# Performance work log

Hardware: AMD Instinct MI355X
Metric: run time of the kernel (lower is better)

The kernel has to match this reference:

```python
import jax, jax.numpy as jnp
import numpy as np

G = 4          # conv groups (hardcoded in module)
C = 1024       # channels (hardcoded cin=cout=1024)
SCALE = 1.0 / np.sqrt(1024.0).astype(np.float32)  # 1/sqrt(c/h), h=1


def grouped_proj(x, W, b):
    # pointwise grouped Conv1d == block-diagonal matmul over channel groups
    # x: [B, C, P], W: [G, C//G out, C//G in], b: [C]
    B, C_, P = x.shape
    xg = x.reshape(B, G, C_ // G, P)
    y = jnp.einsum('goi,bgip->bgop', W, xg)  # [B, G, C//G, P]
    return y.reshape(B, C_, P) + b[None, :, None]


def setup_inputs() -> dict:
    key = jax.random.key(0)
    ks = jax.random.split(key, 8)
    B, PK, PQ = 8, 1024, 4096
    cg = C // G
    w_std = 1.0 / np.sqrt(cg).astype(np.float32)  # ~ conv default init scale
    return {
        'Xq': jax.random.normal(ks[0], (B, C, PQ), jnp.float32),
        'Xk': jax.random.normal(ks[1], (B, C, PK), jnp.float32),
        'Wq': jax.random.normal(ks[2], (G, cg, cg), jnp.float32) * w_std,
        'bq': jax.random.normal(ks[3], (C,), jnp.float32) * 0.01,
        'Wk': jax.random.normal(ks[4], (G, cg, cg), jnp.float32) * w_std,
        'bk': jax.random.normal(ks[5], (C,), jnp.float32) * 0.01,
        'Wv': jax.random.normal(ks[6], (G, cg, cg), jnp.float32) * w_std,
        'bv': jax.random.normal(ks[7], (C,), jnp.float32) * 0.01,
    }


def reference(Xq, Xk, Wq, bq, Wk, bk, Wv, bv):
    # Q and K are both projected from Xk; V from Xq (as in the torch code)
    Q = grouped_proj(Xk, Wq, bq)   # [B, C, Pk]
    K = grouped_proj(Xk, Wk, bk)   # [B, C, Pk]
    V = grouped_proj(Xq, Wv, bv)   # [B, C, Pq]
    b, c, pk = K.shape
    pq = V.shape[-1]
    h = 1
    Qh = Q.reshape(b, h, c // h, pk)
    Kh = K.reshape(b, h, c // h, pk)
    Vh = V.reshape(b, h, c // h, pq)
    # H: [B, h, Pk, Pq], contraction over channels; softmax over dim=-2 (Pk)
    H = jnp.einsum('bhci,bhcj->bhij', Kh, Vh) * SCALE
    H = jax.nn.softmax(H, axis=-2)
    # sparse_constrain: Gram over last axis vs identity, mean squared error
    mid = jnp.einsum('bhci,bhki->bhck', H, H)          # [B, h, Pk, Pk]
    Iden = jnp.eye(pk, dtype=H.dtype)[None, None]       # broadcast over B, h
    sparse_loss = jnp.mean((mid - Iden) ** 2)
    # out: mix Q along Pk with attention H -> [B, h, C, Pq]
    out = jnp.einsum('bhij,bhki->bhkj', H, Qh).reshape(b, c, pq)
    return out, sparse_loss, H
```

## Files before the change

kernel.cpp:

```cpp
#include <hip/hip_runtime.h>

typedef _Float16 f16;
typedef f16 f16x8 __attribute__((ext_vector_type(8)));
typedef float f32x4 __attribute__((ext_vector_type(4)));

__device__ __forceinline__ void gload16(const void* g, void* ldsbase) {
  __builtin_amdgcn_global_load_lds((const __attribute__((address_space(1))) unsigned int*)g,
                                   (__attribute__((address_space(3))) unsigned int*)ldsbase, 16, 0, 0);
}

__device__ __forceinline__ int swz(int row, int c) {
  return row * 64 + ((c ^ ((row >> 1) & 3)) << 4);
}

template<int MODE>
__global__ void __launch_bounds__(512, 2)
gemm256(const f16* __restrict__ A, const f16* __restrict__ Bm, float* __restrict__ Cf,
        f16* __restrict__ E16, f16* __restrict__ E16t,
        int K, long sA, long sB, float scale, float* __restrict__ aux) {
  __shared__ f16 sb[65536];
  const int t = threadIdx.x, l = t & 63, w = t >> 6;
  const int wr = w >> 2, wc = w & 3;
  const int bid = blockIdx.x;
  const int swzb = (bid & 7) * 64 + (bid >> 3);
  const long b = swzb >> 6;
  const int by = (swzb >> 4) & 3, bx = swzb & 15;
  const char* Abyte = (const char*)(A + b * sA + (long)(by * 256) * K);
  const char* Bbyte = (const char*)(Bm + b * sB + (long)(bx * 256) * K);

  int offSrc[4];
#pragma unroll
  for (int i = 0; i < 4; ++i) {
    int cid = i * 512 + t, row = cid >> 3, slot = cid & 7;
    offSrc[i] = row * (K * 2) + ((slot ^ (row & 7)) << 4);
  }
  int offAf[8][2], offBf[4][2];
#pragma unroll
  for (int mi = 0; mi < 8; ++mi) {
    int r = wr * 128 + mi * 16 + (l & 15);
#pragma unroll
    for (int ks = 0; ks < 2; ++ks)
      offAf[mi][ks] = r * 64 + ((((ks << 2) + (l >> 4)) ^ (r & 7)) << 3);
  }
#pragma unroll
  for (int ni = 0; ni < 4; ++ni) {
    int r = wc * 64 + ni * 16 + (l & 15);
#pragma unroll
    for (int ks = 0; ks < 2; ++ks)
      offBf[ni][ks] = r * 64 + ((((ks << 2) + (l >> 4)) ^ (r & 7)) << 3);
  }

  const int NT = K >> 6;
  f32x4 acc[8][4] = {};

  auto STAGE = [&](int kt, int bsel) {
    f16* la = sb + bsel * 32768;
    f16* lb = la + 16384;
    const char* as = Abyte + (long)kt * 128;
    const char* bs = Bbyte + (long)kt * 128;
#pragma unroll
    for (int i = 0; i < 4; ++i)
      gload16(as + offSrc[i], la + (i * 512 + (w << 6)) * 8);
#pragma unroll
    for (int i = 0; i < 4; ++i)
      gload16(bs + offSrc[i], lb + (i * 512 + (w << 6)) * 8);
  };

  STAGE(0, 0);
  for (int kt = 0; kt < NT; ++kt) {
    const int cur = kt & 1;
    if (kt + 1 < NT) {
      STAGE(kt + 1, cur ^ 1);
      asm volatile("s_waitcnt vmcnt(8)" ::: "memory");
    } else {
      asm volatile("s_waitcnt vmcnt(0)" ::: "memory");
    }
    __builtin_amdgcn_s_barrier();
    asm volatile("" ::: "memory");
    const f16* la = sb + cur * 32768;
    const f16* lb = la + 16384;
#pragma unroll
    for (int ks = 0; ks < 2; ++ks) {
      f16x8 bf[4];
#pragma unroll
      for (int ni = 0; ni < 4; ++ni) bf[ni] = *(const f16x8*)(lb + offBf[ni][ks]);
#pragma unroll
      for (int mi = 0; mi < 8; ++mi) {
        f16x8 af = *(const f16x8*)(la + offAf[mi][ks]);
#pragma unroll
        for (int ni = 0; ni < 4; ++ni)
          acc[mi][ni] = __builtin_amdgcn_mfma_f32_16x16x32_f16(af, bf[ni], acc[mi][ni], 0, 0, 0);
      }
    }
    asm volatile("s_waitcnt lgkmcnt(0)" ::: "memory");
    __builtin_amdgcn_s_barrier();
    asm volatile("" ::: "memory");
  }

  const int i0 = by * 256, j0 = bx * 256;
  if (MODE == 2) {
    float csum[4] = {};
#pragma unroll
    for (int mi = 0; mi < 8; ++mi)
#pragma unroll
      for (int ni = 0; ni < 4; ++ni)
#pragma unroll
        for (int q = 0; q < 4; ++q) {
          float e = __expf(acc[mi][ni][q] * scale);
          acc[mi][ni][q] = e;
          csum[ni] += e;
        }
#pragma unroll
    for (int ni = 0; ni < 4; ++ni) {
      csum[ni] += __shfl_xor(csum[ni], 16);
      csum[ni] += __shfl_xor(csum[ni], 32);
    }
    float* colp = (float*)(sb + 34816);
    if (l < 16) {
#pragma unroll
      for (int ni = 0; ni < 4; ++ni) colp[wr * 256 + wc * 64 + ni * 16 + l] = csum[ni];
    }
    __syncthreads();
    if (t < 256) aux[(b * 4 + by) * 4096 + bx * 256 + t] = colp[t] + colp[256 + t];
    f16* E16b = E16 + b * 4194304L;
    f16* E16tb = E16t + b * 4194304L;
#pragma unroll
    for (int s = 0; s < 4; ++s) {
      if (wr == (s >> 1)) {
        const int h = s & 1;
#pragma unroll
        for (int m2 = 0; m2 < 4; ++m2)
#pragma unroll
          for (int ni = 0; ni < 4; ++ni)
#pragma unroll
            for (int q = 0; q < 4; ++q)
              sb[(m2 * 16 + (l >> 4) * 4 + q) * 264 + wc * 64 + ni * 16 + (l & 15)] =
                  (f16)acc[h * 4 + m2][ni][q];
      }
      __syncthreads();
#pragma unroll
      for (int ii = 0; ii < 4; ++ii) {
        int cid = ii * 512 + t, r = cid >> 5, cc = cid & 31;
        *(f16x8*)(E16b + (long)(i0 + s * 64 + r) * 4096 + j0 + cc * 8) =
            *(const f16x8*)(sb + r * 264 + cc * 8);
      }
      const int q4 = w >> 1, r8 = l >> 3, ic = l & 7;
#pragma unroll
      for (int ii = 0; ii < 4; ++ii) {
        int j = q4 * 64 + r8 * 8 + (w & 1) * 4 + ii;
        f16x8 v;
#pragma unroll
        for (int k2 = 0; k2 < 8; ++k2) v[k2] = sb[(ic * 8 + k2) * 264 + j];
        *(f16x8*)(E16tb + (long)(j0 + j) * 1024 + i0 + s * 64 + ic * 8) = v;
      }
      __syncthreads();
    }
  } else {
    const float* ip = aux + b * 4096 + bx * 256 + wc * 64;
    float iv[4];
#pragma unroll
    for (int ni = 0; ni < 4; ++ni) iv[ni] = ip[ni * 16 + (l & 15)];
    float* Cb = Cf + b * 4194304L + (long)(by * 256 + wr * 128) * 4096 + bx * 256 + wc * 64;
#pragma unroll
    for (int mi = 0; mi < 8; ++mi)
#pragma unroll
      for (int ni = 0; ni < 4; ++ni)
#pragma unroll
        for (int q = 0; q < 4; ++q)
          Cb[(long)(mi * 16 + (l >> 4) * 4 + q) * 4096 + ni * 16 + (l & 15)] = acc[mi][ni][q] * iv[ni];
  }
}

__global__ void __launch_bounds__(256, 2)
gram_p(const f16* __restrict__ E, const f16* __restrict__ inv16g, float* __restrict__ parts) {
  __shared__ f16 sb[36864];
  const int t = threadIdx.x, l = t & 63, w = t >> 6, wr = w >> 1, wc = w & 1;
  const int bid = blockIdx.x;
  const int swzb = (bid & 7) * 64 + (bid >> 3);
  const long b = swzb >> 6;
  const int by = (swzb >> 3) & 7, bx = swzb & 7;
  const char* Abyte = (const char*)(E + b * 4194304L + (long)(by * 128) * 4096);
  const char* Bbyte = (const char*)(E + b * 4194304L + (long)(bx * 128) * 4096);
  f16* invl = sb + 32768;
  {
    const char* ig = (const char*)(inv16g + b * 4096);
    gload16(ig + (long)t * 16, invl + (w << 6) * 8);
    gload16(ig + 4096 + (long)t * 16, invl + 2048 + (w << 6) * 8);
  }
  int offSrc[4];
#pragma unroll
  for (int i = 0; i < 4; ++i) {
    int cid = i * 256 + t, row = cid >> 3, slot = cid & 7;
    offSrc[i] = row * 8192 + ((slot ^ (row & 7)) << 4);
  }
  int offA[4][2], offB[4][2];
#pragma unroll
  for (int mi = 0; mi < 4; ++mi) {
    int ra = wr * 64 + mi * 16 + (l & 15);
    int rb = wc * 64 + mi * 16 + (l & 15);
#pragma unroll
    for (int ks = 0; ks < 2; ++ks) {
      offA[mi][ks] = ra * 64 + ((((ks << 2) + (l >> 4)) ^ (ra & 7)) << 3);
      offB[mi][ks] = rb * 64 + ((((ks << 2) + (l >> 4)) ^ (rb & 7)) << 3);
    }
  }
  auto STAGE = [&](int kt, int bsel) {
    f16* la = sb + bsel * 16384;
    f16* lb = la + 8192;
    const char* as = Abyte + (long)kt * 128;
    const char* bs = Bbyte + (long)kt * 128;
#pragma unroll
    for (int i = 0; i < 4; ++i) gload16(as + offSrc[i], la + (i * 256 + (w << 6)) * 8);
#pragma unroll
    for (int i = 0; i < 4; ++i) gload16(bs + offSrc[i], lb + (i * 256 + (w << 6)) * 8);
  };
  f32x4 acc[4][4] = {};
  STAGE(0, 0);
  for (int kt = 0; kt < 64; ++kt) {
    const int cur = kt & 1;
    if (kt + 1 < 64) {
      STAGE(kt + 1, cur ^ 1);
      asm volatile("s_waitcnt vmcnt(8)" ::: "memory");
    } else {
      asm volatile("s_waitcnt vmcnt(0)" ::: "memory");
    }
    __builtin_amdgcn_s_barrier();
    asm volatile("" ::: "memory");
    const f16* la = sb + cur * 16384;
    const f16* lb = la + 8192;
#pragma unroll
    for (int ks = 0; ks < 2; ++ks) {
      const f16x8 invv = *(const f16x8*)(invl + kt * 64 + ks * 32 + ((l >> 4) << 3));
      f16x8 bf[4];
#pragma unroll
      for (int ni = 0; ni < 4; ++ni) bf[ni] = *(const f16x8*)(lb + offB[ni][ks]) * invv;
#pragma unroll
      for (int mi = 0; mi < 4; ++mi) {
        f16x8 af = *(const f16x8*)(la + offA[mi][ks]) * invv;
#pragma unroll
        for (int ni = 0; ni < 4; ++ni)
          acc[mi][ni] = __builtin_amdgcn_mfma_f32_16x16x32_f16(af, bf[ni], acc[mi][ni], 0, 0, 0);
      }
    }
    asm volatile("s_waitcnt lgkmcnt(0)" ::: "memory");
    __builtin_amdgcn_s_barrier();
    asm volatile("" ::: "memory");
  }
  const int gr0 = by * 128 + wr * 64 + (l >> 4) * 4;
  const int gc0 = bx * 128 + wc * 64 + (l & 15);
  float p = 0.f;
#pragma unroll
  for (int mi = 0; mi < 4; ++mi)
#pragma unroll
    for (int ni = 0; ni < 4; ++ni)
#pragma unroll
      for (int q = 0; q < 4; ++q) {
        float e = acc[mi][ni][q];
        if (gr0 + mi * 16 + q == gc0 + ni * 16) e -= 1.f;
        p += e * e;
      }
#pragma unroll
  for (int d = 32; d; d >>= 1) p += __shfl_down(p, d);
  __shared__ float red[4];
  if (l == 0) red[w] = p;
  __syncthreads();
  if (t == 0) parts[bid] = red[0] + red[1] + red[2] + red[3];
}

__global__ void __launch_bounds__(256)
proj_q(const float* __restrict__ X, const f16* __restrict__ W16, const float* __restrict__ bias,
       f16* __restrict__ Q, int P) {
  __shared__ f16 As[4096], Bs[4096];
  const int t = threadIdx.x, l = t & 63, w = t >> 6, wr = w >> 1, wc = w & 1;
  const int bg = blockIdx.z, g = bg & 3;
  const long b = bg >> 2;
  const int p0 = blockIdx.x * 128, m0 = blockIdx.y * 128;
  const float* Xb = X + b * 1024 * P + (long)g * 256 * P;
  const f16* Wg = W16 + g * 65536 + m0 * 256;
  const int r0 = t >> 2, cs = (t & 3) ^ ((r0 >> 1) & 3);
  const f16* wS0 = Wg + r0 * 256 + cs * 8;
  const f16* wS1 = Wg + (r0 + 64) * 256 + cs * 8;
  const int xp = t & 63, xc = t >> 6;
  const float* xS = Xb + (long)(xc * 8) * P + p0 + xp;
  const int xo0 = swz(xp, xc), xo1 = swz(xp + 64, xc);
  int offA[4], offB[4];
#pragma unroll
  for (int i = 0; i < 4; ++i) {
    int ra = wr * 64 + i * 16 + (l & 15);
    offA[i] = swz(ra, l >> 4);
    int rb = wc * 64 + i * 16 + (l & 15);
    offB[i] = swz(rb, l >> 4);
  }
  f32x4 acc[4][4] = {};
  for (int k0 = 0; k0 < 256; k0 += 32) {
    gload16(wS0 + k0, As + w * 512);
    gload16(wS1 + k0, As + 2048 + w * 512);
    const float* xs = xS + (long)k0 * P;
    f16x8 v0, v1;
#pragma unroll
    for (int d = 0; d < 8; ++d) v0[d] = (f16)xs[(long)d * P];
#pragma unroll
    for (int d = 0; d < 8; ++d) v1[d] = (f16)xs[(long)d * P + 64];
    *(f16x8*)((char*)Bs + xo0) = v0;
    *(f16x8*)((char*)Bs + xo1) = v1;
    __syncthreads();
    f16x8 af[4], bf[4];
#pragma unroll
    for (int i = 0; i < 4; ++i) {
      af[i] = *(const f16x8*)((const char*)As + offA[i]);
      bf[i] = *(const f16x8*)((const char*)Bs + offB[i]);
    }
#pragma unroll
    for (int mi = 0; mi < 4; ++mi)
#pragma unroll
      for (int ni = 0; ni < 4; ++ni)
        acc[mi][ni] = __builtin_amdgcn_mfma_f32_16x16x32_f16(af[mi], bf[ni], acc[mi][ni], 0, 0, 0);
    __syncthreads();
  }
  f16* Qb = Q + b * 1048576 + (long)(g * 256 + m0 + wr * 64) * 1024 + p0 + wc * 64;
#pragma unroll
  for (int mi = 0; mi < 4; ++mi)
#pragma unroll
    for (int q = 0; q < 4; ++q) {
      float bv = bias[g * 256 + m0 + wr * 64 + mi * 16 + (l >> 4) * 4 + q];
#pragma unroll
      for (int ni = 0; ni < 4; ++ni)
        Qb[(long)(mi * 16 + (l >> 4) * 4 + q) * 1024 + ni * 16 + (l & 15)] = (f16)(acc[mi][ni][q] + bv);
    }
}

__global__ void __launch_bounds__(256)
proj_kv(const float* __restrict__ X, const f16* __restrict__ W16, const float* __restrict__ bias,
        f16* __restrict__ Yt, int P) {
  __shared__ f16 As[4096], Bs[4096];
  const int t = threadIdx.x, l = t & 63, w = t >> 6, wr = w >> 1, wc = w & 1;
  const int bg = blockIdx.z, g = bg & 3;
  const long b = bg >> 2;
  const int p0 = blockIdx.y * 128, n0 = blockIdx.x * 128;
  const float* Xb = X + b * 1024 * P + (long)g * 256 * P;
  const f16* Wg = W16 + g * 65536 + n0 * 256;
  const int r0 = t >> 2, cs = (t & 3) ^ ((r0 >> 1) & 3);
  const f16* wS0 = Wg + r0 * 256 + cs * 8;
  const f16* wS1 = Wg + (r0 + 64) * 256 + cs * 8;
  const int xp = t & 63, xc = t >> 6;
  const float* xS = Xb + (long)(xc * 8) * P + p0 + xp;
  const int xo0 = swz(xp, xc), xo1 = swz(xp + 64, xc);
  int offA[4], offB[4];
#pragma unroll
  for (int i = 0; i < 4; ++i) {
    int ra = wr * 64 + i * 16 + (l & 15);
    offA[i] = swz(ra, l >> 4);
    int rb = wc * 64 + i * 16 + (l & 15);
    offB[i] = swz(rb, l >> 4);
  }
  f32x4 acc[4][4] = {};
  for (int k0 = 0; k0 < 256; k0 += 32) {
    gload16(wS0 + k0, Bs + w * 512);
    gload16(wS1 + k0, Bs + 2048 + w * 512);
    const float* xs = xS + (long)k0 * P;
    f16x8 v0, v1;
#pragma unroll
    for (int d = 0; d < 8; ++d) v0[d] = (f16)xs[(long)d * P];
#pragma unroll
    for (int d = 0; d < 8; ++d) v1[d] = (f16)xs[(long)d * P + 64];
    *(f16x8*)((char*)As + xo0) = v0;
    *(f16x8*)((char*)As + xo1) = v1;
    __syncthreads();
    f16x8 af[4], bf[4];
#pragma unroll
    for (int i = 0; i < 4; ++i) {
      af[i] = *(const f16x8*)((const char*)As + offA[i]);
      bf[i] = *(const f16x8*)((const char*)Bs + offB[i]);
    }
#pragma unroll
    for (int mi = 0; mi < 4; ++mi)
#pragma unroll
      for (int ni = 0; ni < 4; ++ni)
        acc[mi][ni] = __builtin_amdgcn_mfma_f32_16x16x32_f16(af[mi], bf[ni], acc[mi][ni], 0, 0, 0);
    __syncthreads();
  }
  f16* Yb = Yt + b * P * 1024 + (long)(p0 + wr * 64) * 1024 + g * 256 + n0 + wc * 64;
  float bcol[4];
#pragma unroll
  for (int ni = 0; ni < 4; ++ni) bcol[ni] = bias[g * 256 + n0 + wc * 64 + ni * 16 + (l & 15)];
#pragma unroll
  for (int mi = 0; mi < 4; ++mi)
#pragma unroll
    for (int q = 0; q < 4; ++q)
#pragma unroll
      for (int ni = 0; ni < 4; ++ni)
        Yb[(long)(mi * 16 + (l >> 4) * 4 + q) * 1024 + ni * 16 + (l & 15)] = (f16)(acc[mi][ni][q] + bcol[ni]);
}

__global__ void __launch_bounds__(256)
inv_k(const float* __restrict__ colsum, float* __restrict__ inv, f16* __restrict__ inv16) {
  int gid = blockIdx.x * 256 + threadIdx.x;
  int b = gid >> 12, j = gid & 4095;
  const float* cp = colsum + (long)(b * 4) * 4096 + j;
  float s = 0.f;
#pragma unroll
  for (int my = 0; my < 4; ++my) s += cp[my * 4096];
  float iv = 1.f / s;
  inv[gid] = iv;
  inv16[gid] = (f16)iv;
}

__global__ void __launch_bounds__(256)
h_fin(const f16* __restrict__ E, float* __restrict__ Hf, const float* __restrict__ inv) {
  for (long g = blockIdx.x * 256L + threadIdx.x; g < 33554432L; g += (long)gridDim.x * 256) {
    int b = (int)(g >> 22), j = (int)(g & 4095);
    Hf[g] = (float)E[g] * inv[(b << 12) + j];
  }
}

__global__ void cvt_f16(const float* __restrict__ s, f16* __restrict__ d, int n) {
  int i = blockIdx.x * 256 + threadIdx.x;
  if (i < n) d[i] = (f16)s[i];
}

__global__ void __launch_bounds__(256)
finalize_k(const float* __restrict__ parts, float* __restrict__ o) {
  const int t = threadIdx.x;
  float s = 0.f;
  for (int i = t; i < 512; i += 256) s += parts[i];
#pragma unroll
  for (int d = 32; d; d >>= 1) s += __shfl_down(s, d);
  __shared__ float red[4];
  if ((t & 63) == 0) red[t >> 6] = s;
  __syncthreads();
  if (t == 0) *o = (red[0] + red[1] + red[2] + red[3]) * (1.0f / 8388608.0f);
}

extern "C" void kernel_launch(void* const* d_in, const int* in_sizes, int n_in,
                              void* d_out, int out_size, void* d_ws, size_t ws_size,
                              hipStream_t stream) {
  const float* Xq = (const float*)d_in[0];
  const float* Xk = (const float*)d_in[1];
  const float* Wq = (const float*)d_in[2];
  const float* bq = (const float*)d_in[3];
  const float* Wk = (const float*)d_in[4];
  const float* bk = (const float*)d_in[5];
  const float* Wv = (const float*)d_in[6];
  const float* bv = (const float*)d_in[7];
  float* out = (float*)d_out;
  float* loss_out = out + 33554432;
  float* Hf = out + 33554433;

  char* ws = (char*)d_ws;
  f16* W16q = (f16*)(ws);
  f16* W16k = (f16*)(ws + (1 << 19));
  f16* W16v = (f16*)(ws + 2L * (1 << 19));
  f16* Q16  = (f16*)(ws + 3L * (1 << 19));
  f16* Kt16 = (f16*)(ws + 3L * (1 << 19) + (1L << 24));
  f16* Vt16 = (f16*)(ws + 3L * (1 << 19) + 2L * (1 << 24));
  f16* E16  = (f16*)(ws + 3L * (1 << 19) + 2L * (1 << 24) + (1L << 26));
  f16* E16t = (f16*)(ws + 3L * (1 << 19) + 2L * (1 << 24) + 2L * (1 << 26));
  char* tail = ws + 3L * (1 << 19) + 2L * (1 << 24) + 3L * (1 << 26);
  float* parts = (float*)tail;
  float* invb  = (float*)(tail + 8192);
  f16*   inv16 = (f16*)(tail + 8192 + 131072);
  float* colsum = (float*)(ws);

  cvt_f16<<<1024, 256, 0, stream>>>(Wq, W16q, 262144);
  cvt_f16<<<1024, 256, 0, stream>>>(Wk, W16k, 262144);
  cvt_f16<<<1024, 256, 0, stream>>>(Wv, W16v, 262144);

  proj_q <<<dim3(8, 2, 32), 256, 0, stream>>>(Xk, W16q, bq, Q16, 1024);
  proj_kv<<<dim3(2, 8, 32), 256, 0, stream>>>(Xk, W16k, bk, Kt16, 1024);
  proj_kv<<<dim3(2, 32, 32), 256, 0, stream>>>(Xq, W16v, bv, Vt16, 4096);

  gemm256<2><<<512, 512, 0, stream>>>(Kt16, Vt16, nullptr, E16, E16t,
      1024, 1L << 20, 1L << 22, 0.03125f, colsum);

  inv_k<<<128, 256, 0, stream>>>(colsum, invb, inv16);

  gemm256<3><<<512, 512, 0, stream>>>(Q16, E16t, out, nullptr, nullptr,
      1024, 1L << 20, 1L << 22, 1.0f, invb);

  h_fin<<<2048, 256, 0, stream>>>(E16, Hf, invb);

  gram_p<<<512, 256, 0, stream>>>(E16, inv16, parts);
  finalize_k<<<1, 256, 0, stream>>>(parts, loss_out);
}
```

Before: 419.4 us.

## Fuse Q/K projections, widen projection tiles, vectorize H finalize, merge weight casts

Replaces the separate Q and K projection kernels with one kernel that loads each X tile once and computes both projections. The V projection now uses a full 256-wide output tile per block, so each X element is read once instead of once per output chunk. The three weight cast launches are merged into one, and the H finalize kernel is vectorized four elements at a time. The gram kernel now folds the squared inverse column sum, scaled by 4096, into one operand instead of scaling both, and the gemm block-index mapping is reordered to change L2 reuse. The f16 scaling trick could affect precision of the sparse loss.

```diff
diff --git a/kernel.cpp b/kernel.cpp
--- a/kernel.cpp
+++ b/kernel.cpp
@@ -1,6 +1,7 @@
 #include <hip/hip_runtime.h>
 
 typedef _Float16 f16;
+typedef f16 f16x4 __attribute__((ext_vector_type(4)));
 typedef f16 f16x8 __attribute__((ext_vector_type(8)));
 typedef float f32x4 __attribute__((ext_vector_type(4)));
 
@@ -24,7 +25,8 @@
   const int bid = blockIdx.x;
   const int swzb = (bid & 7) * 64 + (bid >> 3);
   const long b = swzb >> 6;
-  const int by = (swzb >> 4) & 3, bx = swzb & 15;
+  const int inner = swzb & 63;
+  const int bx = inner >> 2, by = inner & 3;
   const char* Abyte = (const char*)(A + b * sA + (long)(by * 256) * K);
   const char* Bbyte = (const char*)(Bm + b * sB + (long)(bx * 256) * K);
 
@@ -172,7 +174,7 @@
 }
 
 __global__ void __launch_bounds__(256, 2)
-gram_p(const f16* __restrict__ E, const f16* __restrict__ inv16g, float* __restrict__ parts) {
+gram_p(const f16* __restrict__ E, const f16* __restrict__ inv2sg, float* __restrict__ parts) {
   __shared__ f16 sb[36864];
   const int t = threadIdx.x, l = t & 63, w = t >> 6, wr = w >> 1, wc = w & 1;
   const int bid = blockIdx.x;
@@ -183,7 +185,7 @@
   const char* Bbyte = (const char*)(E + b * 4194304L + (long)(bx * 128) * 4096);
   f16* invl = sb + 32768;
   {
-    const char* ig = (const char*)(inv16g + b * 4096);
+    const char* ig = (const char*)(inv2sg + b * 4096);
     gload16(ig + (long)t * 16, invl + (w << 6) * 8);
     gload16(ig + 4096 + (long)t * 16, invl + 2048 + (w << 6) * 8);
   }
@@ -233,7 +235,7 @@
       const f16x8 invv = *(const f16x8*)(invl + kt * 64 + ks * 32 + ((l >> 4) << 3));
       f16x8 bf[4];
 #pragma unroll
-      for (int ni = 0; ni < 4; ++ni) bf[ni] = *(const f16x8*)(lb + offB[ni][ks]) * invv;
+      for (int ni = 0; ni < 4; ++ni) bf[ni] = *(const f16x8*)(lb + offB[ni][ks]);
 #pragma unroll
       for (int mi = 0; mi < 4; ++mi) {
         f16x8 af = *(const f16x8*)(la + offA[mi][ks]) * invv;
@@ -255,7 +257,7 @@
     for (int ni = 0; ni < 4; ++ni)
 #pragma unroll
       for (int q = 0; q < 4; ++q) {
-        float e = acc[mi][ni][q];
+        float e = acc[mi][ni][q] * (1.0f / 4096.0f);
         if (gr0 + mi * 16 + q == gc0 + ni * 16) e -= 1.f;
         p += e * e;
       }
@@ -267,133 +269,160 @@
   if (t == 0) parts[bid] = red[0] + red[1] + red[2] + red[3];
 }
 
-__global__ void __launch_bounds__(256)
-proj_q(const float* __restrict__ X, const f16* __restrict__ W16, const float* __restrict__ bias,
-       f16* __restrict__ Q, int P) {
-  __shared__ f16 As[4096], Bs[4096];
-  const int t = threadIdx.x, l = t & 63, w = t >> 6, wr = w >> 1, wc = w & 1;
+__global__ void __launch_bounds__(512)
+proj_qk(const float* __restrict__ X, const f16* __restrict__ Wq16, const f16* __restrict__ Wk16,
+        const float* __restrict__ bq, const float* __restrict__ bk,
+        f16* __restrict__ Q, f16* __restrict__ Kt) {
+  __shared__ f16 sb[20480];
+  f16* Wqs = sb;
+  f16* Wks = sb + 8192;
+  f16* Xs = sb + 16384;
+  const int t = threadIdx.x, l = t & 63, w = t >> 6;
+  const int wrq = w >> 1, wcq = w & 1;
   const int bg = blockIdx.z, g = bg & 3;
   const long b = bg >> 2;
-  const int p0 = blockIdx.x * 128, m0 = blockIdx.y * 128;
-  const float* Xb = X + b * 1024 * P + (long)g * 256 * P;
-  const f16* Wg = W16 + g * 65536 + m0 * 256;
-  const int r0 = t >> 2, cs = (t & 3) ^ ((r0 >> 1) & 3);
-  const f16* wS0 = Wg + r0 * 256 + cs * 8;
-  const f16* wS1 = Wg + (r0 + 64) * 256 + cs * 8;
-  const int xp = t & 63, xc = t >> 6;
-  const float* xS = Xb + (long)(xc * 8) * P + p0 + xp;
-  const int xo0 = swz(xp, xc), xo1 = swz(xp + 64, xc);
-  int offA[4], offB[4];
+  const int p0 = blockIdx.x * 128;
+  const float* Xb = X + b * 1048576 + (long)g * 262144;
+  const char* WqB = (const char*)(Wq16 + g * 65536);
+  const char* WkB = (const char*)(Wk16 + g * 65536);
+  int wOff[2];
+#pragma unroll
+  for (int i = 0; i < 2; ++i) {
+    int c = i * 512 + t, row = c >> 2, slot = (c & 3) ^ ((row >> 1) & 3);
+    wOff[i] = row * 512 + (slot << 4);
+  }
+  const int xp = t & 127, xc = t >> 7;
+  const float* xS = Xb + (long)(xc * 8) * 1024 + p0 + xp;
+  const int xo = swz(xp, xc);
+  int offW[4], offX[4];
 #pragma unroll
   for (int i = 0; i < 4; ++i) {
-    int ra = wr * 64 + i * 16 + (l & 15);
-    offA[i] = swz(ra, l >> 4);
-    int rb = wc * 64 + i * 16 + (l & 15);
-    offB[i] = swz(rb, l >> 4);
+    int rc = wrq * 64 + i * 16 + (l & 15);
+    offW[i] = swz(rc, l >> 4);
+    int rp = wcq * 64 + i * 16 + (l & 15);
+    offX[i] = swz(rp, l >> 4);
+  }
+  f32x4 accq[4][4] = {}, acck[4][4] = {};
+  for (int k0 = 0; k0 < 256; k0 += 32) {
+#pragma unroll
+    for (int i = 0; i < 2; ++i) {
+      gload16(WqB + wOff[i] + k0 * 2, Wqs + (i * 512 + (w << 6)) * 8);
+      gload16(WkB + wOff[i] + k0 * 2, Wks + (i * 512 + (w << 6)) * 8);
+    }
+    const float* xs = xS + (long)k0 * 1024;
+    f16x8 v;
+#pragma unroll
+    for (int d = 0; d < 8; ++d) v[d] = (f16)xs[(long)d * 1024];
+    *(f16x8*)((char*)Xs + xo) = v;
+    __syncthreads();
+    f16x8 qf[4], kf[4], xf[4];
+#pragma unroll
+    for (int i = 0; i < 4; ++i) {
+      qf[i] = *(const f16x8*)((const char*)Wqs + offW[i]);
+      kf[i] = *(const f16x8*)((const char*)Wks + offW[i]);
+      xf[i] = *(const f16x8*)((const char*)Xs + offX[i]);
+    }
+#pragma unroll
+    for (int mi = 0; mi < 4; ++mi)
+#pragma unroll
+      for (int ni = 0; ni < 4; ++ni) {
+        accq[mi][ni] = __builtin_amdgcn_mfma_f32_16x16x32_f16(qf[mi], xf[ni], accq[mi][ni], 0, 0, 0);
+        acck[ni][mi] = __builtin_amdgcn_mfma_f32_16x16x32_f16(xf[ni], kf[mi], acck[ni][mi], 0, 0, 0);
+      }
+    __syncthreads();
+  }
+  f16* Qb = Q + b * 1048576 + (long)(g * 256 + wrq * 64) * 1024 + p0 + wcq * 64;
+#pragma unroll
+  for (int mi = 0; mi < 4; ++mi)
+#pragma unroll
+    for (int q = 0; q < 4; ++q) {
+      float bv = bq[g * 256 + wrq * 64 + mi * 16 + (l >> 4) * 4 + q];
+#pragma unroll
+      for (int ni = 0; ni < 4; ++ni)
+        Qb[(long)(mi * 16 + (l >> 4) * 4 + q) * 1024 + ni * 16 + (l & 15)] = (f16)(accq[mi][ni][q] + bv);
+    }
+  f16* Kb = Kt + b * 1048576 + (long)(p0 + wcq * 64) * 1024 + g * 256 + wrq * 64;
+  float bcol[4];
+#pragma unroll
+  for (int ni = 0; ni < 4; ++ni) bcol[ni] = bk[g * 256 + wrq * 64 + ni * 16 + (l & 15)];
+#pragma unroll
+  for (int mi = 0; mi < 4; ++mi)
+#pragma unroll
+    for (int q = 0; q < 4; ++q)
+#pragma unroll
+      for (int ni = 0; ni < 4; ++ni)
+        Kb[(long)(mi * 16 + (l >> 4) * 4 + q) * 1024 + ni * 16 + (l & 15)] = (f16)(acck[mi][ni][q] + bcol[ni]);
+}
+
+__global__ void __launch_bounds__(512)
+proj_v(const float* __restrict__ X, const f16* __restrict__ Wv16, const float* __restrict__ bv,
+       f16* __restrict__ Vt) {
+  __shared__ f16 sb[12288];
+  f16* Wvs = sb;
+  f16* Xs = sb + 8192;
+  const int t = threadIdx.x, l = t & 63, w = t >> 6;
+  const int wrq = w >> 1, wcq = w & 1;
+  const int bg = blockIdx.z, g = bg & 3;
+  const long b = bg >> 2;
+  const int p0 = blockIdx.x * 128;
+  const float* Xb = X + b * 4194304 + (long)g * 1048576;
+  const char* WvB = (const char*)(Wv16 + g * 65536);
+  int wOff[2];
+#pragma unroll
+  for (int i = 0; i < 2; ++i) {
+    int c = i * 512 + t, row = c >> 2, slot = (c & 3) ^ ((row >> 1) & 3);
+    wOff[i] = row * 512 + (slot << 4);
+  }
+  const int xp = t & 127, xc = t >> 7;
+  const float* xS = Xb + (long)(xc * 8) * 4096 + p0 + xp;
+  const int xo = swz(xp, xc);
+  int offW[4], offX[4];
+#pragma unroll
+  for (int i = 0; i < 4; ++i) {
+    int rc = wrq * 64 + i * 16 + (l & 15);
+    offW[i] = swz(rc, l >> 4);
+    int rp = wcq * 64 + i * 16 + (l & 15);
+    offX[i] = swz(rp, l >> 4);
   }
   f32x4 acc[4][4] = {};
   for (int k0 = 0; k0 < 256; k0 += 32) {
-    gload16(wS0 + k0, As + w * 512);
-    gload16(wS1 + k0, As + 2048 + w * 512);
-    const float* xs = xS + (long)k0 * P;
-    f16x8 v0, v1;
-#pragma unroll
-    for (int d = 0; d < 8; ++d) v0[d] = (f16)xs[(long)d * P];
-#pragma unroll
-    for (int d = 0; d < 8; ++d) v1[d] = (f16)xs[(long)d * P + 64];
-    *(f16x8*)((char*)Bs + xo0) = v0;
-    *(f16x8*)((char*)Bs + xo1) = v1;
+#pragma unroll
+    for (int i = 0; i < 2; ++i)
+      gload16(WvB + wOff[i] + k0 * 2, Wvs + (i * 512 + (w << 6)) * 8);
+    const float* xs = xS + (long)k0 * 4096;
+    f16x8 v;
+#pragma unroll
+    for (int d = 0; d < 8; ++d) v[d] = (f16)xs[(long)d * 4096];
+    *(f16x8*)((char*)Xs + xo) = v;
     __syncthreads();
-    f16x8 af[4], bf[4];
+    f16x8 wf[4], xf[4];
 #pragma unroll
     for (int i = 0; i < 4; ++i) {
-      af[i] = *(const f16x8*)((const char*)As + offA[i]);
-      bf[i] = *(const f16x8*)((const char*)Bs + offB[i]);
+      wf[i] = *(const f16x8*)((const char*)Wvs + offW[i]);
+      xf[i] = *(const f16x8*)((const char*)Xs + offX[i]);
     }
 #pragma unroll
     for (int mi = 0; mi < 4; ++mi)
 #pragma unroll
       for (int ni = 0; ni < 4; ++ni)
-        acc[mi][ni] = __builtin_amdgcn_mfma_f32_16x16x32_f16(af[mi], bf[ni], acc[mi][ni], 0, 0, 0);
+        acc[mi][ni] = __builtin_amdgcn_mfma_f32_16x16x32_f16(xf[mi], wf[ni], acc[mi][ni], 0, 0, 0);
     __syncthreads();
   }
-  f16* Qb = Q + b * 1048576 + (long)(g * 256 + m0 + wr * 64) * 1024 + p0 + wc * 64;
+  f16* Vb = Vt + b * 4194304 + (long)(p0 + wcq * 64) * 1024 + g * 256 + wrq * 64;
+  float bcol[4];
+#pragma unroll
+  for (int ni = 0; ni < 4; ++ni) bcol[ni] = bv[g * 256 + wrq * 64 + ni * 16 + (l & 15)];
 #pragma unroll
   for (int mi = 0; mi < 4; ++mi)
 #pragma unroll
-    for (int q = 0; q < 4; ++q) {
-      float bv = bias[g * 256 + m0 + wr * 64 + mi * 16 + (l >> 4) * 4 + q];
+    for (int q = 0; q < 4; ++q)
 #pragma unroll
       for (int ni = 0; ni < 4; ++ni)
-        Qb[(long)(mi * 16 + (l >> 4) * 4 + q) * 1024 + ni * 16 + (l & 15)] = (f16)(acc[mi][ni][q] + bv);
-    }
+        Vb[(long)(mi * 16 + (l >> 4) * 4 + q) * 1024 + ni * 16 + (l & 15)] = (f16)(acc[mi][ni][q] + bcol[ni]);
 }
 
 __global__ void __launch_bounds__(256)
-proj_kv(const float* __restrict__ X, const f16* __restrict__ W16, const float* __restrict__ bias,
-        f16* __restrict__ Yt, int P) {
-  __shared__ f16 As[4096], Bs[4096];
-  const int t = threadIdx.x, l = t & 63, w = t >> 6, wr = w >> 1, wc = w & 1;
-  const int bg = blockIdx.z, g = bg & 3;
-  const long b = bg >> 2;
-  const int p0 = blockIdx.y * 128, n0 = blockIdx.x * 128;
-  const float* Xb = X + b * 1024 * P + (long)g * 256 * P;
-  const f16* Wg = W16 + g * 65536 + n0 * 256;
-  const int r0 = t >> 2, cs = (t & 3) ^ ((r0 >> 1) & 3);
-  const f16* wS0 = Wg + r0 * 256 + cs * 8;
-  const f16* wS1 = Wg + (r0 + 64) * 256 + cs * 8;
-  const int xp = t & 63, xc = t >> 6;
-  const float* xS = Xb + (long)(xc * 8) * P + p0 + xp;
-  const int xo0 = swz(xp, xc), xo1 = swz(xp + 64, xc);
-  int offA[4], offB[4];
-#pragma unroll
-  for (int i = 0; i < 4; ++i) {
-    int ra = wr * 64 + i * 16 + (l & 15);
-    offA[i] = swz(ra, l >> 4);
-    int rb = wc * 64 + i * 16 + (l & 15);
-    offB[i] = swz(rb, l >> 4);
-  }
-  f32x4 acc[4][4] = {};
-  for (int k0 = 0; k0 < 256; k0 += 32) {
-    gload16(wS0 + k0, Bs + w * 512);
-    gload16(wS1 + k0, Bs + 2048 + w * 512);
-    const float* xs = xS + (long)k0 * P;
-    f16x8 v0, v1;
-#pragma unroll
-    for (int d = 0; d < 8; ++d) v0[d] = (f16)xs[(long)d * P];
-#pragma unroll
-    for (int d = 0; d < 8; ++d) v1[d] = (f16)xs[(long)d * P + 64];
-    *(f16x8*)((char*)As + xo0) = v0;
-    *(f16x8*)((char*)As + xo1) = v1;
-    __syncthreads();
-    f16x8 af[4], bf[4];
-#pragma unroll
-    for (int i = 0; i < 4; ++i) {
-      af[i] = *(const f16x8*)((const char*)As + offA[i]);
-      bf[i] = *(const f16x8*)((const char*)Bs + offB[i]);
-    }
-#pragma unroll
-    for (int mi = 0; mi < 4; ++mi)
-#pragma unroll
-      for (int ni = 0; ni < 4; ++ni)
-        acc[mi][ni] = __builtin_amdgcn_mfma_f32_16x16x32_f16(af[mi], bf[ni], acc[mi][ni], 0, 0, 0);
-    __syncthreads();
-  }
-  f16* Yb = Yt + b * P * 1024 + (long)(p0 + wr * 64) * 1024 + g * 256 + n0 + wc * 64;
-  float bcol[4];
-#pragma unroll
-  for (int ni = 0; ni < 4; ++ni) bcol[ni] = bias[g * 256 + n0 + wc * 64 + ni * 16 + (l & 15)];
-#pragma unroll
-  for (int mi = 0; mi < 4; ++mi)
-#pragma unroll
-    for (int q = 0; q < 4; ++q)
-#pragma unroll
-      for (int ni = 0; ni < 4; ++ni)
-        Yb[(long)(mi * 16 + (l >> 4) * 4 + q) * 1024 + ni * 16 + (l & 15)] = (f16)(acc[mi][ni][q] + bcol[ni]);
-}
-
-__global__ void __launch_bounds__(256)
-inv_k(const float* __restrict__ colsum, float* __restrict__ inv, f16* __restrict__ inv16) {
+inv_k(const float* __restrict__ colsum, float* __restrict__ inv, f16* __restrict__ inv2s) {
   int gid = blockIdx.x * 256 + threadIdx.x;
   int b = gid >> 12, j = gid & 4095;
   const float* cp = colsum + (long)(b * 4) * 4096 + j;
@@ -402,20 +431,32 @@
   for (int my = 0; my < 4; ++my) s += cp[my * 4096];
   float iv = 1.f / s;
   inv[gid] = iv;
-  inv16[gid] = (f16)iv;
+  inv2s[gid] = (f16)(iv * iv * 4096.0f);
 }
 
 __global__ void __launch_bounds__(256)
 h_fin(const f16* __restrict__ E, float* __restrict__ Hf, const float* __restrict__ inv) {
-  for (long g = blockIdx.x * 256L + threadIdx.x; g < 33554432L; g += (long)gridDim.x * 256) {
-    int b = (int)(g >> 22), j = (int)(g & 4095);
-    Hf[g] = (float)E[g] * inv[(b << 12) + j];
-  }
-}
-
-__global__ void cvt_f16(const float* __restrict__ s, f16* __restrict__ d, int n) {
+  for (long g = blockIdx.x * 256L + threadIdx.x; g < 8388608L; g += (long)gridDim.x * 256) {
+    long i4 = g * 4;
+    int b = (int)(i4 >> 22), j = (int)(i4 & 4095);
+    f16x4 e = *(const f16x4*)(E + i4);
+    f32x4 iv = *(const f32x4*)(inv + (b << 12) + j);
+    float* hp = Hf + i4;
+    hp[0] = (float)e[0] * iv[0];
+    hp[1] = (float)e[1] * iv[1];
+    hp[2] = (float)e[2] * iv[2];
+    hp[3] = (float)e[3] * iv[3];
+  }
+}
+
+__global__ void cvt3(const float* __restrict__ a, const float* __restrict__ b2,
+                     const float* __restrict__ c, f16* __restrict__ da,
+                     f16* __restrict__ db, f16* __restrict__ dc) {
   int i = blockIdx.x * 256 + threadIdx.x;
-  if (i < n) d[i] = (f16)s[i];
+  int which = i >> 18, r = i & 262143;
+  if (which == 0) da[r] = (f16)a[r];
+  else if (which == 1) db[r] = (f16)b2[r];
+  else dc[r] = (f16)c[r];
 }
 
 __global__ void __launch_bounds__(256)
@@ -458,27 +499,24 @@
   char* tail = ws + 3L * (1 << 19) + 2L * (1 << 24) + 3L * (1 << 26);
   float* parts = (float*)tail;
   float* invb  = (float*)(tail + 8192);
-  f16*   inv16 = (f16*)(tail + 8192 + 131072);
+  f16*   inv2s = (f16*)(tail + 8192 + 131072);
   float* colsum = (float*)(ws);
 
-  cvt_f16<<<1024, 256, 0, stream>>>(Wq, W16q, 262144);
-  cvt_f16<<<1024, 256, 0, stream>>>(Wk, W16k, 262144);
-  cvt_f16<<<1024, 256, 0, stream>>>(Wv, W16v, 262144);
-
-  proj_q <<<dim3(8, 2, 32), 256, 0, stream>>>(Xk, W16q, bq, Q16, 1024);
-  proj_kv<<<dim3(2, 8, 32), 256, 0, stream>>>(Xk, W16k, bk, Kt16, 1024);
-  proj_kv<<<dim3(2, 32, 32), 256, 0, stream>>>(Xq, W16v, bv, Vt16, 4096);
+  cvt3<<<3072, 256, 0, stream>>>(Wq, Wk, Wv, W16q, W16k, W16v);
+
+  proj_qk<<<dim3(8, 1, 32), 512, 0, stream>>>(Xk, W16q, W16k, bq, bk, Q16, Kt16);
+  proj_v <<<dim3(32, 1, 32), 512, 0, stream>>>(Xq, W16v, bv, Vt16);
 
   gemm256<2><<<512, 512, 0, stream>>>(Kt16, Vt16, nullptr, E16, E16t,
       1024, 1L << 20, 1L << 22, 0.03125f, colsum);
 
-  inv_k<<<128, 256, 0, stream>>>(colsum, invb, inv16);
+  inv_k<<<128, 256, 0, stream>>>(colsum, invb, inv2s);
 
   gemm256<3><<<512, 512, 0, stream>>>(Q16, E16t, out, nullptr, nullptr,
       1024, 1L << 20, 1L << 22, 1.0f, invb);
 
   h_fin<<<2048, 256, 0, stream>>>(E16, Hf, invb);
 
-  gram_p<<<512, 256, 0, stream>>>(E16, inv16, parts);
+  gram_p<<<512, 256, 0, stream>>>(E16, inv2s, parts);
   finalize_k<<<1, 256, 0, stream>>>(parts, loss_out);
 }
```

After: 385.1 us. 8.2% less time.
